# Kernel tuning notes

Hardware: AMD Instinct MI355X
Metric: run time of the kernel (lower is better)

## Reference

```python
import jax, jax.numpy as jnp
import numpy as np

# Static trigram-LM trie configuration (uniform branching K per node).
V_ = 32000; N_ = 3; K_ = 32; S_ = 32; SOS_ = 0; B_ = 32; L_ = 8
U_ = V_ + 1
N_BI = V_ * K_                    # number of bigram nodes
O_ = U_ + N_BI + 1                # offsets/logbs length (bigram block + sentinel)
N_TRI = N_BI * K_                 # number of trigram leaves
G_ = N_TRI
P_ = O_ + G_                      # logps length


def _build_trie():
    """Valid CSR-style flattened trie: children of node at position q live at
    [offsets[q]+q, offsets[q+1]+q+1); every node has exactly K children with
    sorted token ids 0..K-1. ids[p-U_] is the token id of node at position p."""
    rng = np.random.default_rng(0)
    offsets = np.empty(O_, np.int64)
    # unigram v's children occupy positions [U_+v*K_, U_+(v+1)*K_)
    offsets[:U_] = U_ + np.arange(U_) * (K_ - 1)
    # bigram j (position U_+j) children occupy [O_+j*K_, O_+(j+1)*K_)
    offsets[U_:] = (O_ - U_) + np.arange(N_BI + 1) * (K_ - 1)
    ids = np.empty(P_ - U_, np.int32)
    ids[:N_BI] = np.arange(N_BI) % K_       # bigram node token ids
    ids[N_BI] = 0                           # sentinel slot at position O_-1
    ids[N_BI + 1:] = np.arange(N_TRI) % K_  # trigram leaf token ids
    logps = (-rng.uniform(0.1, 10.0, P_)).astype(np.float32)
    logbs = (-rng.uniform(0.01, 2.0, O_)).astype(np.float32)
    return offsets.astype(np.int32), ids, logps, logbs


def setup_inputs() -> dict:
    key = jax.random.key(0)
    k1, k2 = jax.random.split(key)
    offsets, ids, logps, logbs = _build_trie()
    # tokens in [0, 2K): half of them miss in the trie -> exercises backoff path
    hist = jax.random.randint(k1, (L_, B_), 0, 2 * K_, dtype=jnp.int32)
    hidx = jax.random.randint(k2, (B_,), 0, L_, dtype=jnp.int32)
    return {"hist": hist, "hidx": hidx, "offsets": jnp.asarray(offsets),
            "ids": jnp.asarray(ids), "logps": jnp.asarray(logps),
            "logbs": jnp.asarray(logbs), "sos": SOS_, "V": V_, "N": N_,
            "G": G_, "S": S_}


def reference(hist, hidx, offsets, ids, logps, logbs, sos, V, N, G, S):
    B = hist.shape[1]
    M = B * V
    O = offsets.shape[0]
    P = logps.shape[0]
    shift = 0 if 0 <= sos < V else 1
    U = V + shift + 1 % N
    if N == 1:
        return jnp.broadcast_to(logps[:V], (B, V))
    # Always left-pad N-1 sos tokens (equivalent to torch's rem padding; the
    # subsequent window gather makes extra padding harmless).
    pad = N - 1
    hist = jnp.concatenate([jnp.full((pad, B), sos, hist.dtype), hist])
    hidx = hidx + pad
    # context = the N-1 tokens at positions hidx-(N-1) .. hidx-1, per batch
    pos = hidx[None, :] - (N - 1) + jnp.arange(N - 1)[:, None]   # (N-1, B)
    ctx = jnp.take_along_axis(hist, pos, axis=0)                  # (N-1, B)
    if shift:
        ctx = jnp.where(ctx == sos, V, ctx)
    ctx = ctx.astype(ids.dtype)
    srange = jnp.arange(S)
    # first M entries: candidate words v per batch; last B: context pointer
    desc = jnp.concatenate([jnp.tile(jnp.arange(V, dtype=jnp.int32), B),
                            ctx[-1].astype(jnp.int32)])
    last_logps = jnp.tile(logps[:V], B)                           # (M,)
    last_backoffs = jnp.repeat(logbs[desc[M:]], V)                # (M,)
    found = jnp.ones(M + B, bool)
    for n in range(1, N):
        hist_n = jnp.concatenate([jnp.repeat(ctx[-n], V), ctx[-min(n + 1, N - 1)]])
        desc_starts = offsets[desc] + desc
        desc_ends = offsets[desc + 1] + desc + 1
        pos_desc = desc_starts[:, None] + srange[None, :]         # (M+B, S)
        ext = desc_ends[:, None] > pos_desc
        ids_ = ids[jnp.minimum(pos_desc, P - 1) - U]
        ext = ext & (hist_n[:, None] == ids_)
        found = ext.any(1) & found
        desc = jnp.where(found, jnp.where(ext, pos_desc, 0).sum(1), desc)
        logps_desc = logps[desc[:M]]
        if n == N - 1:
            cur_backoffs = jnp.zeros_like(last_backoffs)
        else:
            cur_backoffs = jnp.repeat(
                jnp.where(found[M:], logbs[jnp.minimum(desc[M:], O - 1)], 0.0), V)
        clobber = jnp.isfinite(logps_desc) & found[:M]
        cur_logps = jnp.where(clobber, logps_desc,
                              last_logps + cur_backoffs + last_backoffs)
        last_backoffs = jnp.where(clobber, cur_backoffs, 0.0)
        last_logps = jnp.where(jnp.repeat(hidx >= n, V), cur_logps, last_logps)
    return last_logps.reshape(B, V)
```

## Files before the change

### kernel.cpp

```cpp
#include <hip/hip_runtime.h>
#include <math.h>


#define MAXN 8
#define BG   16
#define WI   37
#define WO   41

struct PerB {
  int   ctx[MAXN];
  float bo[MAXN];
  float b1;
  int   hp;
};

__device__ __forceinline__ bool find_child(const int* __restrict__ offsets,
                                           const int* __restrict__ ids,
                                           int q, int t, int U, int P, int S,
                                           int* pos_out) {
  int start = offsets[q] + q;
  int end   = offsets[q + 1] + q + 1;
  int n = end - start;
  if (n > S) n = S;
  if (n <= 0) return false;
  int j = (t < n - 1) ? t : (n - 1);
  if (j < 0) j = 0;
  int x = ids[min(start + j, P - 1) - U];
  if (x == t) { *pos_out = start + j; return true; }
  if (x < t) return false;
  int lo = 0, hi = j - 1;
  while (lo < hi) {
    int mid = (lo + hi) >> 1;
    int xm = ids[min(start + mid, P - 1) - U];
    if (xm < t) lo = mid + 1; else hi = mid;
  }
  if (lo < j) {
    int xm = ids[min(start + lo, P - 1) - U];
    if (xm == t) { *pos_out = start + lo; return true; }
  }
  return false;
}

__global__ void lm_prep(const int* __restrict__ hist, const int* __restrict__ hidx,
                        const int* __restrict__ offsets, const int* __restrict__ ids,
                        const float* __restrict__ logbs,
                        const int* __restrict__ sos_p, const int* __restrict__ N_p,
                        const int* __restrict__ S_p,
                        PerB* __restrict__ pb, int V, int B, int L, int O, int P) {
  int b = blockIdx.x * blockDim.x + threadIdx.x;
  if (b >= B) return;
  int sos = *sos_p, N = *N_p, S = *S_p;
  if (N <= 1) return;
  int shift = (0 <= sos && sos < V) ? 0 : 1;
  int U = V + shift + 1 % N;
  int pad = N - 1;
  int hp = hidx[b] + pad;
  PerB o;
  o.hp = hp;
  for (int k = 0; k < N - 1; ++k) {
    int r = hp - (N - 1) + k;
    int tok = (r < pad) ? sos : hist[(r - pad) * B + b];
    if (shift && tok == sos) tok = V;
    o.ctx[k] = tok;
  }
  o.b1 = logbs[o.ctx[N - 2]];
  int desc = o.ctx[N - 2];
  bool found = true;
  for (int n = 1; n <= N - 2; ++n) {
    int t = o.ctx[(N - 1) - min(n + 1, N - 1)];
    if (found) {
      int pos;
      found = find_child(offsets, ids, desc, t, U, P, S, &pos);
      if (found) desc = pos;
    }
    o.bo[n] = found ? logbs[min(desc, O - 1)] : 0.0f;
  }
  pb[b] = o;
}

__device__ __forceinline__ float score_v(const int* __restrict__ offsets,
                                         const int* __restrict__ ids,
                                         const float* __restrict__ logps,
                                         const PerB* __restrict__ pbb,
                                         int v, float lp0,
                                         int N, int U, int O, int P, int S) {
  float last_lp = lp0;
  float last_bo = pbb->b1;
  int hp = pbb->hp;
  int desc = v;
  bool found = true;
  float cur_lp = lp0;
  for (int n = 1; n <= N - 1; ++n) {
    int t = pbb->ctx[(N - 1) - n];
    if (found) {
      int pos;
      found = find_child(offsets, ids, desc, t, U, P, S, &pos);
      if (found) { desc = pos; cur_lp = logps[desc]; }
    }
    float cur_bo = (n == N - 1) ? 0.0f : pbb->bo[n];
    bool clobber = isfinite(cur_lp) && found;
    float newlp = clobber ? cur_lp : (last_lp + cur_bo + last_bo);
    last_bo = clobber ? cur_bo : 0.0f;
    if (hp >= n) last_lp = newlp;
  }
  return last_lp;
}

__global__ void __launch_bounds__(64)
lm_main2(const int* __restrict__ offsets, const int* __restrict__ ids,
         const float* __restrict__ logps,
         const int* __restrict__ sos_p, const int* __restrict__ N_p,
         const int* __restrict__ S_p,
         const PerB* __restrict__ pb, float* __restrict__ out,
         int V, int B, int O, int P) {
  __shared__ int   s_t1[BG], s_t0[BG], s_hp[BG];
  __shared__ float s_bo1[BG], s_b1[BG];
  __shared__ int   ids_w[64 * WI];
  __shared__ int   off_w[64 * WO];

  const int tid = threadIdx.x;
  const int v   = blockIdx.x * 64 + tid;
  const int b0  = blockIdx.y * BG;
  const int N = *N_p, S = *S_p, sos = *sos_p;
  const int Nc = (N > 0) ? N : 1;
  const int shift = (0 <= sos && sos < V) ? 0 : 1;
  const int U = V + shift + 1 % Nc;

  const bool fast = (N == 3) && (S == 32);

  if (!fast) {
    if (v < V) {
      float lp0 = logps[v];
      if (N <= 1) {
        for (int i = 0; i < BG; ++i) {
          int b = b0 + i;
          if (b < B) out[(size_t)b * V + v] = lp0;
        }
      } else {
        for (int i = 0; i < BG; ++i) {
          int b = b0 + i;
          if (b < B)
            out[(size_t)b * V + v] = score_v(offsets, ids, logps, pb + b, v,
                                             lp0, N, U, O, P, S);
        }
      }
    }
    return;
  }

  if (tid < BG) {
    int b = b0 + tid;
    if (b < B) {
      const PerB* q = pb + b;
      s_t1[tid]  = q->ctx[1];
      s_t0[tid]  = q->ctx[0];
      s_bo1[tid] = q->bo[1];
      s_b1[tid]  = q->b1;
      s_hp[tid]  = q->hp;
    }
  }
  __syncthreads();
  if (v >= V) return;

  const int idsN = P - U;
  float lp0 = logps[v];
  int ov  = offsets[v];
  int ov1 = offsets[v + 1];
  int start1 = ov + v;
  int n1 = ov1 + 1 - ov;
  if (n1 > 32) n1 = 32;

  int* myids = ids_w + tid * WI;
  int* myoff = off_w + tid * WO;
  int aidx0 = start1 - U;
  int sh_i = 0, sh_o = 0;
  bool vec_ok = (start1 >= 0) && (aidx0 >= 0) &&
                (((aidx0 & ~3) + 36) <= idsN) &&
                (((start1 & ~3) + 40) <= O);
  if (vec_ok) {
    int ab = aidx0 & ~3;
    sh_i = aidx0 - ab;
    const int4* ip = (const int4*)(ids + ab);
#pragma unroll
    for (int k = 0; k < 9; ++k) {
      int4 t = ip[k];
      myids[4 * k + 0] = t.x; myids[4 * k + 1] = t.y;
      myids[4 * k + 2] = t.z; myids[4 * k + 3] = t.w;
    }
    int ob = start1 & ~3;
    sh_o = start1 - ob;
    const int4* op = (const int4*)(offsets + ob);
#pragma unroll
    for (int k = 0; k < 10; ++k) {
      int4 t = op[k];
      myoff[4 * k + 0] = t.x; myoff[4 * k + 1] = t.y;
      myoff[4 * k + 2] = t.z; myoff[4 * k + 3] = t.w;
    }
  } else {
    for (int j = 0; j < 36; ++j) {
      int ii = min(start1 + j, P - 1) - U;
      ii = max(0, min(ii, idsN - 1));
      myids[j] = ids[ii];
    }
    for (int j = 0; j < 40; ++j) {
      int oo = max(0, min(start1 + j, O - 1));
      myoff[j] = offsets[oo];
    }
  }

  const int nb = min(BG, B - b0);

  int j1v[BG];
  int cc1[BG];
  int cc2[BG];
  unsigned f1m = 0, l2m = 0;
#pragma unroll
  for (int i = 0; i < BG; ++i) {
    if (i >= nb) { j1v[i] = 0; cc1[i] = v; cc2[i] = v; continue; }
    int t1 = s_t1[i];
    bool found = false;
    int j1 = 0;
    if (n1 > 0) {
      int jj = (t1 < n1 - 1) ? t1 : (n1 - 1);
      if (jj < 0) jj = 0;
      int x = myids[sh_i + jj];
      if (x == t1) { found = true; j1 = jj; }
      else if (x > t1) {
        int lo = 0, hi = jj - 1;
        while (lo < hi) {
          int mid = (lo + hi) >> 1;
          if (myids[sh_i + mid] < t1) lo = mid + 1; else hi = mid;
        }
        if (lo < jj && myids[sh_i + lo] == t1) { found = true; j1 = lo; }
      }
    }
    int c1 = start1 + j1;
    j1v[i] = j1;
    int a1 = min(c1, P - 1);
    cc1[i] = a1;
    int t0 = s_t0[i];
    int o1 = myoff[sh_o + j1];
    int o2 = myoff[sh_o + j1 + 1];
    int start2 = o1 + c1;
    int n2 = o2 + 1 - o1;
    if (n2 > 32) n2 = 32;
    bool l2ok = found && (n2 > 0);
    int jj2 = (t0 < n2 - 1) ? t0 : (n2 - 1);
    if (jj2 < 0) jj2 = 0;
    int c2 = min(start2 + jj2, P - 1);
    cc2[i] = l2ok ? c2 : a1;
    f1m |= (found ? 1u : 0u) << i;
    l2m |= (l2ok ? 1u : 0u) << i;
  }

  float lp1v[BG];
  int   x2v[BG];
  float sp2v[BG];
#pragma unroll
  for (int i = 0; i < BG; ++i) lp1v[i] = logps[cc1[i]];
#pragma unroll
  for (int i = 0; i < BG; ++i) {
    int ii = cc2[i] - U;
    ii = max(0, min(ii, idsN - 1));
    x2v[i] = __builtin_nontemporal_load(ids + ii);
  }
#pragma unroll
  for (int i = 0; i < BG; ++i)
    sp2v[i] = __builtin_nontemporal_load(logps + cc2[i]);

#pragma unroll
  for (int i = 0; i < BG; ++i) {
    if (i >= nb) continue;
    bool found = (f1m >> i) & 1u;
    bool l2ok  = (l2m >> i) & 1u;
    int   hp = s_hp[i];
    float bo1 = s_bo1[i];
    float last_bo = s_b1[i];
    float last_lp = lp0;

    float lp1 = found ? lp1v[i] : lp0;
    bool clob = found && isfinite(lp1);
    float nl = clob ? lp1 : (last_lp + bo1 + last_bo);
    last_bo = clob ? bo1 : 0.0f;
    if (hp >= 1) last_lp = nl;

    bool f2 = false;
    float lp2 = 0.0f;
    if (l2ok) {
      int t0 = s_t0[i];
      int x2 = x2v[i];
      if (x2 == t0) { f2 = true; lp2 = sp2v[i]; }
      else if (x2 > t0) {
        int j1 = j1v[i];
        int c1 = start1 + j1;
        int o1 = myoff[sh_o + j1];
        int o2 = myoff[sh_o + j1 + 1];
        int start2 = o1 + c1;
        int n2 = o2 + 1 - o1;
        if (n2 > 32) n2 = 32;
        int jj2 = (t0 < n2 - 1) ? t0 : (n2 - 1);
        if (jj2 < 0) jj2 = 0;
        int lo = 0, hi = jj2 - 1;
        while (lo < hi) {
          int mid = (lo + hi) >> 1;
          int im = max(0, min(min(start2 + mid, P - 1) - U, idsN - 1));
          if (ids[im] < t0) lo = mid + 1; else hi = mid;
        }
        if (lo < jj2) {
          int il = max(0, min(min(start2 + lo, P - 1) - U, idsN - 1));
          if (ids[il] == t0) { f2 = true; lp2 = logps[min(start2 + lo, P - 1)]; }
        }
      }
    }
    bool clob2 = f2 && isfinite(lp2);
    float nl2 = clob2 ? lp2 : (last_lp + last_bo);
    if (hp >= 2) last_lp = nl2;

    __builtin_nontemporal_store(last_lp, out + (size_t)(b0 + i) * V + v);
  }
}

extern "C" void kernel_launch(void* const* d_in, const int* in_sizes, int n_in,
                              void* d_out, int out_size, void* d_ws, size_t ws_size,
                              hipStream_t stream) {
  const int*   hist    = (const int*)d_in[0];
  const int*   hidx    = (const int*)d_in[1];
  const int*   offsets = (const int*)d_in[2];
  const int*   ids     = (const int*)d_in[3];
  const float* logps   = (const float*)d_in[4];
  const float* logbs   = (const float*)d_in[5];
  const int*   sos_p   = (const int*)d_in[6];
  const int*   N_p     = (const int*)d_in[8];
  const int*   S_p     = (const int*)d_in[10];

  int B = in_sizes[1];
  int L = in_sizes[0] / B;
  int O = in_sizes[2];
  int P = in_sizes[4];
  int V = out_size / B;
  float* out = (float*)d_out;
  PerB* pb = (PerB*)d_ws;

  lm_prep<<<dim3((B + 63) / 64), dim3(64), 0, stream>>>(
      hist, hidx, offsets, ids, logbs, sos_p, N_p, S_p, pb, V, B, L, O, P);

  dim3 grid((V + 63) / 64, (B + BG - 1) / BG);
  lm_main2<<<grid, dim3(64), 0, stream>>>(
      offsets, ids, logps, sos_p, N_p, S_p, pb, out, V, B, O, P);
}
```

Baseline: 275.5 us.

## Share per-v trie window across four waves covering all batch rows

Blocks grow from one wave to four waves, and each block now covers all 32 batch rows for 64 vocabulary entries instead of 16 rows. The per-v unigram child ids and offsets windows are loaded once into shared memory cooperatively, four threads per row, and then reused by all four waves. Each wave handles 8 batch rows. This halves redundant reloads of the unigram windows across batch groups and spreads the load work over more threads. In exchange it uses more shared memory per block and adds a block-wide sync before compute.

```diff
diff --git a/kernel.cpp b/kernel.cpp
--- a/kernel.cpp
+++ b/kernel.cpp
@@ -3,7 +3,8 @@
 
 
 #define MAXN 8
-#define BG   16
+#define BGW  8
+#define BGB  32
 #define WI   37
 #define WO   41
 
@@ -106,21 +107,25 @@
   return last_lp;
 }
 
-__global__ void __launch_bounds__(64)
-lm_main2(const int* __restrict__ offsets, const int* __restrict__ ids,
+__global__ void __launch_bounds__(256)
+lm_main3(const int* __restrict__ offsets, const int* __restrict__ ids,
          const float* __restrict__ logps,
          const int* __restrict__ sos_p, const int* __restrict__ N_p,
          const int* __restrict__ S_p,
          const PerB* __restrict__ pb, float* __restrict__ out,
          int V, int B, int O, int P) {
-  __shared__ int   s_t1[BG], s_t0[BG], s_hp[BG];
-  __shared__ float s_bo1[BG], s_b1[BG];
+  __shared__ int   s_t1[BGB], s_t0[BGB], s_hp[BGB];
+  __shared__ float s_bo1[BGB], s_b1[BGB];
   __shared__ int   ids_w[64 * WI];
   __shared__ int   off_w[64 * WO];
-
-  const int tid = threadIdx.x;
-  const int v   = blockIdx.x * 64 + tid;
-  const int b0  = blockIdx.y * BG;
+  __shared__ int   s_start1[64], s_n1[64], s_shi[64], s_sho[64];
+
+  const int tid  = threadIdx.x;
+  const int lane = tid & 63;
+  const int w    = tid >> 6;
+  const int vbase = blockIdx.x * 64;
+  const int v     = vbase + lane;
+  const int b0    = blockIdx.y * BGB;
   const int N = *N_p, S = *S_p, sos = *sos_p;
   const int Nc = (N > 0) ? N : 1;
   const int shift = (0 <= sos && sos < V) ? 0 : 1;
@@ -132,13 +137,13 @@
     if (v < V) {
       float lp0 = logps[v];
       if (N <= 1) {
-        for (int i = 0; i < BG; ++i) {
-          int b = b0 + i;
+        for (int ib = w; ib < BGB; ib += 4) {
+          int b = b0 + ib;
           if (b < B) out[(size_t)b * V + v] = lp0;
         }
       } else {
-        for (int i = 0; i < BG; ++i) {
-          int b = b0 + i;
+        for (int ib = w; ib < BGB; ib += 4) {
+          int b = b0 + ib;
           if (b < B)
             out[(size_t)b * V + v] = score_v(offsets, ids, logps, pb + b, v,
                                              lp0, N, U, O, P, S);
@@ -148,7 +153,7 @@
     return;
   }
 
-  if (tid < BG) {
+  if (tid < BGB) {
     int b = b0 + tid;
     if (b < B) {
       const PerB* q = pb + b;
@@ -159,65 +164,84 @@
       s_hp[tid]  = q->hp;
     }
   }
+
+  const int idsN = P - U;
+
+  {
+    int row  = tid >> 2;
+    int part = tid & 3;
+    int vv = vbase + row;
+    if (vv < V) {
+      int ov  = offsets[vv];
+      int ov1 = offsets[vv + 1];
+      int start1 = ov + vv;
+      int n1 = ov1 + 1 - ov;
+      if (n1 > 32) n1 = 32;
+      int* myids = ids_w + row * WI;
+      int* myoff = off_w + row * WO;
+      int aidx0 = start1 - U;
+      int sh_i = 0, sh_o = 0;
+      bool vec_ok = (start1 >= 0) && (aidx0 >= 0) &&
+                    (((aidx0 & ~3) + 36) <= idsN) &&
+                    (((start1 & ~3) + 40) <= O);
+      if (vec_ok) {
+        int ab = aidx0 & ~3;
+        sh_i = aidx0 - ab;
+        const int4* ip = (const int4*)(ids + ab);
+        for (int k = part; k < 9; k += 4) {
+          int4 t = ip[k];
+          myids[4 * k + 0] = t.x; myids[4 * k + 1] = t.y;
+          myids[4 * k + 2] = t.z; myids[4 * k + 3] = t.w;
+        }
+        int ob = start1 & ~3;
+        sh_o = start1 - ob;
+        const int4* op = (const int4*)(offsets + ob);
+        for (int k = part; k < 10; k += 4) {
+          int4 t = op[k];
+          myoff[4 * k + 0] = t.x; myoff[4 * k + 1] = t.y;
+          myoff[4 * k + 2] = t.z; myoff[4 * k + 3] = t.w;
+        }
+      } else {
+        for (int j = part; j < 36; j += 4) {
+          int ii = min(start1 + j, P - 1) - U;
+          ii = max(0, min(ii, idsN - 1));
+          myids[j] = ids[ii];
+        }
+        for (int j = part; j < 40; j += 4) {
+          int oo = max(0, min(start1 + j, O - 1));
+          myoff[j] = offsets[oo];
+        }
+      }
+      if (part == 0) {
+        s_start1[row] = start1; s_n1[row] = n1;
+        s_shi[row] = sh_i;      s_sho[row] = sh_o;
+      }
+    } else if (part == 0) {
+      s_start1[row] = 0; s_n1[row] = 0; s_shi[row] = 0; s_sho[row] = 0;
+    }
+  }
   __syncthreads();
   if (v >= V) return;
 
-  const int idsN = P - U;
   float lp0 = logps[v];
-  int ov  = offsets[v];
-  int ov1 = offsets[v + 1];
-  int start1 = ov + v;
-  int n1 = ov1 + 1 - ov;
-  if (n1 > 32) n1 = 32;
-
-  int* myids = ids_w + tid * WI;
-  int* myoff = off_w + tid * WO;
-  int aidx0 = start1 - U;
-  int sh_i = 0, sh_o = 0;
-  bool vec_ok = (start1 >= 0) && (aidx0 >= 0) &&
-                (((aidx0 & ~3) + 36) <= idsN) &&
-                (((start1 & ~3) + 40) <= O);
-  if (vec_ok) {
-    int ab = aidx0 & ~3;
-    sh_i = aidx0 - ab;
-    const int4* ip = (const int4*)(ids + ab);
-#pragma unroll
-    for (int k = 0; k < 9; ++k) {
-      int4 t = ip[k];
-      myids[4 * k + 0] = t.x; myids[4 * k + 1] = t.y;
-      myids[4 * k + 2] = t.z; myids[4 * k + 3] = t.w;
-    }
-    int ob = start1 & ~3;
-    sh_o = start1 - ob;
-    const int4* op = (const int4*)(offsets + ob);
-#pragma unroll
-    for (int k = 0; k < 10; ++k) {
-      int4 t = op[k];
-      myoff[4 * k + 0] = t.x; myoff[4 * k + 1] = t.y;
-      myoff[4 * k + 2] = t.z; myoff[4 * k + 3] = t.w;
-    }
-  } else {
-    for (int j = 0; j < 36; ++j) {
-      int ii = min(start1 + j, P - 1) - U;
-      ii = max(0, min(ii, idsN - 1));
-      myids[j] = ids[ii];
-    }
-    for (int j = 0; j < 40; ++j) {
-      int oo = max(0, min(start1 + j, O - 1));
-      myoff[j] = offsets[oo];
-    }
-  }
-
-  const int nb = min(BG, B - b0);
-
-  int j1v[BG];
-  int cc1[BG];
-  int cc2[BG];
+  const int start1 = s_start1[lane];
+  const int n1     = s_n1[lane];
+  const int sh_i   = s_shi[lane];
+  const int sh_o   = s_sho[lane];
+  const int* myids = ids_w + lane * WI;
+  const int* myoff = off_w + lane * WO;
+
+  const int nb = min(BGB, B - b0);
+
+  int j1v[BGW];
+  int cc1[BGW];
+  int cc2[BGW];
   unsigned f1m = 0, l2m = 0;
 #pragma unroll
-  for (int i = 0; i < BG; ++i) {
-    if (i >= nb) { j1v[i] = 0; cc1[i] = v; cc2[i] = v; continue; }
-    int t1 = s_t1[i];
+  for (int i = 0; i < BGW; ++i) {
+    int ib = w * BGW + i;
+    if (ib >= nb) { j1v[i] = 0; cc1[i] = v; cc2[i] = v; continue; }
+    int t1 = s_t1[ib];
     bool found = false;
     int j1 = 0;
     if (n1 > 0) {
@@ -238,7 +262,7 @@
     j1v[i] = j1;
     int a1 = min(c1, P - 1);
     cc1[i] = a1;
-    int t0 = s_t0[i];
+    int t0 = s_t0[ib];
     int o1 = myoff[sh_o + j1];
     int o2 = myoff[sh_o + j1 + 1];
     int start2 = o1 + c1;
@@ -253,29 +277,30 @@
     l2m |= (l2ok ? 1u : 0u) << i;
   }
 
-  float lp1v[BG];
-  int   x2v[BG];
-  float sp2v[BG];
-#pragma unroll
-  for (int i = 0; i < BG; ++i) lp1v[i] = logps[cc1[i]];
-#pragma unroll
-  for (int i = 0; i < BG; ++i) {
+  float lp1v[BGW];
+  int   x2v[BGW];
+  float sp2v[BGW];
+#pragma unroll
+  for (int i = 0; i < BGW; ++i) lp1v[i] = logps[cc1[i]];
+#pragma unroll
+  for (int i = 0; i < BGW; ++i) {
     int ii = cc2[i] - U;
     ii = max(0, min(ii, idsN - 1));
     x2v[i] = __builtin_nontemporal_load(ids + ii);
   }
 #pragma unroll
-  for (int i = 0; i < BG; ++i)
+  for (int i = 0; i < BGW; ++i)
     sp2v[i] = __builtin_nontemporal_load(logps + cc2[i]);
 
 #pragma unroll
-  for (int i = 0; i < BG; ++i) {
-    if (i >= nb) continue;
+  for (int i = 0; i < BGW; ++i) {
+    int ib = w * BGW + i;
+    if (ib >= nb) continue;
     bool found = (f1m >> i) & 1u;
     bool l2ok  = (l2m >> i) & 1u;
-    int   hp = s_hp[i];
-    float bo1 = s_bo1[i];
-    float last_bo = s_b1[i];
+    int   hp = s_hp[ib];
+    float bo1 = s_bo1[ib];
+    float last_bo = s_b1[ib];
     float last_lp = lp0;
 
     float lp1 = found ? lp1v[i] : lp0;
@@ -287,7 +312,7 @@
     bool f2 = false;
     float lp2 = 0.0f;
     if (l2ok) {
-      int t0 = s_t0[i];
+      int t0 = s_t0[ib];
       int x2 = x2v[i];
       if (x2 == t0) { f2 = true; lp2 = sp2v[i]; }
       else if (x2 > t0) {
@@ -316,7 +341,7 @@
     float nl2 = clob2 ? lp2 : (last_lp + last_bo);
     if (hp >= 2) last_lp = nl2;
 
-    __builtin_nontemporal_store(last_lp, out + (size_t)(b0 + i) * V + v);
+    __builtin_nontemporal_store(last_lp, out + (size_t)(b0 + ib) * V + v);
   }
 }
 
@@ -344,7 +369,7 @@
   lm_prep<<<dim3((B + 63) / 64), dim3(64), 0, stream>>>(
       hist, hidx, offsets, ids, logbs, sos_p, N_p, S_p, pb, V, B, L, O, P);
 
-  dim3 grid((V + 63) / 64, (B + BG - 1) / BG);
-  lm_main2<<<grid, dim3(64), 0, stream>>>(
+  dim3 grid((V + 63) / 64, (B + BGB - 1) / BGB);
+  lm_main3<<<grid, dim3(256), 0, stream>>>(
       offsets, ids, logps, sos_p, N_p, S_p, pb, out, V, B, O, P);
 }
```

Result: no change. 271.3 us (-1.5%).
